# Performance work log

Hardware: AMD Instinct MI355X
Metric: run time of the kernel (lower is better)

## Reference

```python
import jax, jax.numpy as jnp
import numpy as np
import math

B, S, D = 2, 2048, 1024
N_HEAD = 16
EPS = 1e-6

def setup_inputs() -> dict:
    key = jax.random.key(0)
    ks = jax.random.split(key, 12)
    def lin(k):
        kw, kb = jax.random.split(k)
        scale = 1.0 / math.sqrt(D)
        W = jax.random.uniform(kw, (D, D), jnp.float32, -scale, scale)
        b = jax.random.uniform(kb, (D,), jnp.float32, -scale, scale)
        return W, b
    Wq, bq = lin(ks[0]); Wk, bk = lin(ks[1]); Wv, bv = lin(ks[2]); Wo, bo = lin(ks[3])
    return {
        'query': jax.random.normal(ks[4], (B, S, D), jnp.float32),
        'key':   jax.random.normal(ks[5], (B, S, D), jnp.float32),
        'value': jax.random.normal(ks[6], (B, S, D), jnp.float32),
        'mask':  jnp.ones((B, S, S), jnp.int32),
        'Wq': Wq, 'bq': bq, 'Wk': Wk, 'bk': bk, 'Wv': Wv, 'bv': bv,
        'Wo': Wo, 'bo': bo,
        'gamma': jnp.ones((D,), jnp.float32),
        'beta':  jnp.zeros((D,), jnp.float32),
    }

def reference(query, key, value, mask, Wq, bq, Wk, bk, Wv, bv, Wo, bo, gamma, beta):
    b, s, dm = query.shape
    h = N_HEAD
    d = dm // h
    residual = query
    # projections (torch Linear: x @ W.T + b) -> [b, h, s, d]
    def proj(x, W, bias):
        return (x @ W.T + bias).reshape(b, -1, h, d).transpose(0, 2, 1, 3)
    q = proj(query, Wq, bq)
    k = proj(key, Wk, bk)
    v = proj(value, Wv, bv)
    scores = jnp.einsum('bhqd,bhkd->bhqk', q, k) / jnp.sqrt(jnp.float32(d))
    scores = jnp.where(mask[:, None, :, :] == 0, jnp.float32(-1e9), scores)
    p_attn = jax.nn.softmax(scores, axis=-1)  # dropout is identity in eval/reference
    x = jnp.einsum('bhqk,bhkd->bhqd', p_attn, v)
    x = x.transpose(0, 2, 1, 3).reshape(b, -1, h * d)
    x = x @ Wo.T + bo
    x = x + residual
    # LayerNorm with unbiased std and (std + eps) denominator, as in source
    mean = jnp.mean(x, axis=-1, keepdims=True)
    std = jnp.std(x, axis=-1, keepdims=True, ddof=1)
    return gamma * (x - mean) / (std + EPS) + beta
```

## Files before the change

kernel.cpp:

```cpp
#include <hip/hip_runtime.h>
#include <hip/hip_bf16.h>
#include <math.h>
#include <stdint.h>

#define BATCH 2
#define SEQ   2048
#define DMODEL 1024
#define NHEAD 16
#define HDIM  64
#define NROWS (BATCH*SEQ)
#define EPS   1e-6f
#define QSCALE 0.1803368801111204f

typedef float f32x4 __attribute__((ext_vector_type(4)));
typedef short s16x8 __attribute__((ext_vector_type(8)));

#define OFF_XQ 0
#define OFF_XK 4194304
#define OFF_XV 8388608
#define OFF_WQ 12582912
#define OFF_WK 13631488
#define OFF_WV 14680064
#define OFF_WO 15728640
#define OFF_QB 16777216
#define OFF_KB 20971520
#define OFF_VT 25165824
#define OFF_CM 29360128
#define OFF_MS 29884416

__device__ __forceinline__ unsigned short f2bf(float x) {
    unsigned int u = __builtin_bit_cast(unsigned int, x);
    u += 0x7fff + ((u >> 16) & 1);
    return (unsigned short)(u >> 16);
}

__device__ __forceinline__ void gl_lds16(const void* g, void* l) {
    __builtin_amdgcn_global_load_lds(
        (const __attribute__((address_space(1))) unsigned int*)g,
        (__attribute__((address_space(3))) unsigned int*)(unsigned int)(unsigned long long)l,
        16, 0, 0);
}

__global__ __launch_bounds__(256) void conv_all_kernel(
    const float* __restrict__ q, const float* __restrict__ k, const float* __restrict__ v,
    const float* __restrict__ wq, const float* __restrict__ wk, const float* __restrict__ wv,
    const float* __restrict__ wo, unsigned short* __restrict__ ws)
{
    if (blockIdx.x == 0 && threadIdx.x < 32)
        ((unsigned int*)(ws + OFF_MS))[threadIdx.x] = 0;
    size_t t = ((size_t)blockIdx.x * 256 + threadIdx.x) * 4;
    const float* src; unsigned short* dst; size_t off;
    if (t < 4194304)       { src = q;  dst = ws + OFF_XQ; off = t; }
    else if (t < 8388608)  { src = k;  dst = ws + OFF_XK; off = t - 4194304; }
    else if (t < 12582912) { src = v;  dst = ws + OFF_XV; off = t - 8388608; }
    else if (t < 13631488) { src = wq; dst = ws + OFF_WQ; off = t - 12582912; }
    else if (t < 14680064) { src = wk; dst = ws + OFF_WK; off = t - 13631488; }
    else if (t < 15728640) { src = wv; dst = ws + OFF_WV; off = t - 14680064; }
    else                   { src = wo; dst = ws + OFF_WO; off = t - 15728640; }
    float4 x = *(const float4*)&src[off];
    ushort4 o;
    o.x = f2bf(x.x); o.y = f2bf(x.y); o.z = f2bf(x.z); o.w = f2bf(x.w);
    *(ushort4*)&dst[off] = o;
}

__global__ __launch_bounds__(256) void mask_compress_kernel(
    const int* __restrict__ mask, unsigned long long* __restrict__ cm,
    unsigned int* __restrict__ msum)
{
    int t = blockIdx.x * 256 + threadIdx.x;
    int s  = t & 2047;
    int kb = (t >> 11) & 31;
    int b  = t >> 16;
    const int* mp = mask + ((size_t)b * SEQ + s) * SEQ + kb * 64;
    unsigned long long bits = 0;
    #pragma unroll
    for (int i = 0; i < 16; i++) {
        int4 m4 = *(const int4*)&mp[i * 4];
        unsigned long long nib =
            (unsigned long long)((m4.x != 0) | ((m4.y != 0) << 1) |
                                 ((m4.z != 0) << 2) | ((m4.w != 0) << 3));
        bits |= nib << (i * 4);
    }
    cm[((size_t)b * 32 + kb) * SEQ + s] = bits;
    if (bits != ~0ull)
        atomicOr(&msum[(b << 4) | (s >> 7)], 1u << kb);
}

__device__ __forceinline__ void gemm_body(
    const unsigned short* A, const unsigned short* W, int r0, int c0,
    unsigned short* As, unsigned short* Bs, f32x4 acc[4][4])
{
    const int tid  = threadIdx.x;
    const int wave = tid >> 6, lane = tid & 63;
    const int quad = lane >> 4, l15 = lane & 15;
    const int wr = wave >> 1, wc = wave & 1;
    for (int k0 = 0; k0 < DMODEL; k0 += 64) {
        __syncthreads();
        #pragma unroll
        for (int r = 0; r < 4; r++) {
            int f   = r * 4096 + tid * 16;
            int row = f >> 7;
            int g   = (((f >> 4) & 7) - row) & 7;
            gl_lds16((const char*)A + (size_t)(r0 + row) * 2048 + k0 * 2 + g * 16,
                     (char*)As + r * 4096 + wave * 1024);
            gl_lds16((const char*)W + (size_t)(c0 + row) * 2048 + k0 * 2 + g * 16,
                     (char*)Bs + r * 4096 + wave * 1024);
        }
        __syncthreads();
        #pragma unroll
        for (int ks = 0; ks < 2; ks++) {
            s16x8 a[4], b[4];
            #pragma unroll
            for (int mt = 0; mt < 4; mt++) {
                int row = wr*64 + mt*16 + l15;
                a[mt] = *(const s16x8*)((const char*)As + row * 128 + ((ks*4 + quad + row) & 7) * 16);
            }
            #pragma unroll
            for (int nt = 0; nt < 4; nt++) {
                int row = wc*64 + nt*16 + l15;
                b[nt] = *(const s16x8*)((const char*)Bs + row * 128 + ((ks*4 + quad + row) & 7) * 16);
            }
            #pragma unroll
            for (int mt = 0; mt < 4; mt++)
                #pragma unroll
                for (int nt = 0; nt < 4; nt++)
                    acc[mt][nt] = __builtin_amdgcn_mfma_f32_16x16x32_bf16(a[mt], b[nt], acc[mt][nt], 0, 0, 0);
        }
    }
}

__global__ __launch_bounds__(256) void qkv_gemm_kernel(
    unsigned short* __restrict__ ws,
    const float* __restrict__ bq, const float* __restrict__ bk, const float* __restrict__ bv)
{
    __shared__ __align__(16) unsigned short As[8192];
    __shared__ __align__(16) unsigned short Bs[8192];
    const int z = blockIdx.z;
    const unsigned short *A, *W;
    int r0, c0;
    if (z != 2) {
        A = ws + (size_t)z * 4194304;
        W = ws + OFF_WQ + (size_t)z * 1048576;
        r0 = blockIdx.x * 128; c0 = blockIdx.y * 128;
    } else {
        A = ws + OFF_WV;
        W = ws + OFF_XV;
        r0 = blockIdx.y * 128; c0 = blockIdx.x * 128;
    }
    const float* bias = (z == 0) ? bq : (z == 1 ? bk : bv);
    unsigned short* outp = ws + OFF_QB + (size_t)z * 4194304;
    const float scale = (z == 0) ? QSCALE : 1.0f;

    f32x4 acc[4][4] = {};
    gemm_body(A, W, r0, c0, As, Bs, acc);

    const int lane = threadIdx.x & 63, wave = threadIdx.x >> 6;
    const int quad = lane >> 4, l15 = lane & 15;
    const int wr = wave >> 1, wc = wave & 1;
    if (z != 2) {
        float bias_v[4];
        #pragma unroll
        for (int nt = 0; nt < 4; nt++) bias_v[nt] = bias[c0 + wc*64 + nt*16 + l15];
        #pragma unroll
        for (int mt = 0; mt < 4; mt++) {
            #pragma unroll
            for (int nt = 0; nt < 4; nt++) {
                int c = c0 + wc*64 + nt*16 + l15;
                int hh = c >> 6, dd = c & 63;
                #pragma unroll
                for (int reg = 0; reg < 4; reg++) {
                    int r = r0 + wr*64 + mt*16 + quad*4 + reg;
                    int bb = r >> 11, ss = r & (SEQ - 1);
                    float val = (acc[mt][nt][reg] + bias_v[nt]) * scale;
                    outp[(((size_t)(bb*NHEAD + hh)) * SEQ + ss) * HDIM + dd] = f2bf(val);
                }
            }
        }
    } else {
        #pragma unroll
        for (int mt = 0; mt < 4; mt++) {
            #pragma unroll
            for (int reg = 0; reg < 4; reg++) {
                int f = r0 + wr*64 + mt*16 + quad*4 + reg;
                int hh = f >> 6, dd = f & 63;
                float bfv = bias[f];
                #pragma unroll
                for (int nt = 0; nt < 4; nt++) {
                    int r = c0 + wc*64 + nt*16 + l15;
                    int bb = r >> 11, ss = r & (SEQ - 1);
                    outp[(((size_t)(bb*NHEAD + hh)) * HDIM + dd) * SEQ + ss] =
                        f2bf(acc[mt][nt][reg] + bfv);
                }
            }
        }
    }
}

__global__ __launch_bounds__(256) void oproj_gemm_kernel(
    const unsigned short* __restrict__ ws, const float* __restrict__ bo,
    const float* __restrict__ resid, float* __restrict__ outf)
{
    __shared__ __align__(16) unsigned short As[8192];
    __shared__ __align__(16) unsigned short Bs[8192];
    const unsigned short* A = ws + OFF_XQ;
    const unsigned short* W = ws + OFF_WO;
    const int r0 = blockIdx.x * 128, c0 = blockIdx.y * 128;

    f32x4 acc[4][4] = {};
    gemm_body(A, W, r0, c0, (unsigned short*)As, (unsigned short*)Bs, acc);

    const int lane = threadIdx.x & 63, wave = threadIdx.x >> 6;
    const int quad = lane >> 4, l15 = lane & 15;
    const int wr = wave >> 1, wc = wave & 1;
    #pragma unroll
    for (int mt = 0; mt < 4; mt++) {
        #pragma unroll
        for (int nt = 0; nt < 4; nt++) {
            int c = c0 + wc*64 + nt*16 + l15;
            float bv = bo[c];
            #pragma unroll
            for (int reg = 0; reg < 4; reg++) {
                int r = r0 + wr*64 + mt*16 + quad*4 + reg;
                size_t idx = (size_t)r * DMODEL + c;
                outf[idx] = acc[mt][nt][reg] + bv + resid[idx];
            }
        }
    }
}

__global__ __launch_bounds__(512) void attn_mfma_kernel(
    const unsigned short* __restrict__ ws,
    const unsigned long long* __restrict__ cmask,
    const unsigned int* __restrict__ msum,
    unsigned short* __restrict__ ab)
{
    const int tid  = threadIdx.x;
    const int wave = tid >> 6, lane = tid & 63;
    const int quad = lane >> 4, l15 = lane & 15;
    const int h = blockIdx.y, b = blockIdx.z;
    const int qw = blockIdx.x * 128 + wave * 16;

    const char* qh = (const char*)(ws + OFF_QB + ((size_t)(b*NHEAD + h)) * SEQ * HDIM);
    const char* kh = (const char*)(ws + OFF_KB + ((size_t)(b*NHEAD + h)) * SEQ * HDIM);
    const char* vh = (const char*)(ws + OFF_VT + ((size_t)(b*NHEAD + h)) * SEQ * HDIM);

    __shared__ __align__(16) char Ks[2][8192];
    __shared__ __align__(16) char Vs[2][8192];
    __shared__ __align__(16) unsigned short Pl[8][16 * 72];
    unsigned short* Pw = Pl[wave];

    const unsigned int chunkflags = msum[(b << 4) | blockIdx.x];

    const int srow = tid >> 3;
    const int sgrp = ((tid & 7) - srow) & 7;

    #define STAGE(bf, k0)                                                       \
        do {                                                                    \
            gl_lds16(kh + (size_t)((k0) + srow) * 128 + sgrp * 16,              \
                     Ks[bf] + wave * 1024);                                     \
            gl_lds16(vh + (size_t)srow * 4096 + (size_t)(k0) * 2 + sgrp * 16,   \
                     Vs[bf] + wave * 1024);                                     \
        } while (0)

    s16x8 qa[2];
    #pragma unroll
    for (int ks = 0; ks < 2; ks++)
        qa[ks] = *(const s16x8*)(qh + (size_t)(qw + l15) * 128 + ks*64 + quad*16);

    s16x8 onesf;
    {
        short so = (short)0x3F80;
        if (l15 == 0) onesf = (s16x8){so, so, so, so, so, so, so, so};
        else          onesf = (s16x8){0, 0, 0, 0, 0, 0, 0, 0};
    }

    f32x4 o[4], lsum = {0.f, 0.f, 0.f, 0.f};
    #pragma unroll
    for (int nt = 0; nt < 4; nt++) o[nt] = (f32x4){0.f, 0.f, 0.f, 0.f};

    STAGE(0, 0);
    int bf = 0;
    for (int k0 = 0; k0 < SEQ; k0 += 64) {
        __syncthreads();
        if (k0 + 64 < SEQ) STAGE(bf ^ 1, k0 + 64);

        const char* Kb = Ks[bf];
        const char* Vb = Vs[bf];
        f32x4 s[4];
        #pragma unroll
        for (int nt = 0; nt < 4; nt++) {
            int key = nt*16 + l15;
            s16x8 kf0 = *(const s16x8*)(Kb + key*128 + ((quad     + key) & 7) * 16);
            s16x8 kf1 = *(const s16x8*)(Kb + key*128 + ((4 + quad + key) & 7) * 16);
            f32x4 z = {0.f, 0.f, 0.f, 0.f};
            s[nt] = __builtin_amdgcn_mfma_f32_16x16x32_bf16(qa[0], kf0, z, 0, 0, 0);
            s[nt] = __builtin_amdgcn_mfma_f32_16x16x32_bf16(qa[1], kf1, s[nt], 0, 0, 0);
        }
        if (chunkflags & (1u << (k0 >> 6))) {
            const unsigned long long* cmp =
                cmask + ((size_t)b*32 + (k0 >> 6)) * SEQ + qw + quad*4;
            #pragma unroll
            for (int reg = 0; reg < 4; reg++) {
                unsigned long long cm = cmp[reg];
                if (cm != ~0ull) {
                    #pragma unroll
                    for (int nt = 0; nt < 4; nt++) {
                        int n = nt*16 + l15;
                        if (!((cm >> n) & 1)) s[nt][reg] = -1e9f;
                    }
                }
            }
        }
        #pragma unroll
        for (int nt = 0; nt < 4; nt++)
            #pragma unroll
            for (int reg = 0; reg < 4; reg++) {
                float pv = exp2f(s[nt][reg]);
                Pw[(quad*4 + reg) * 72 + nt*16 + l15] =
                    (unsigned short)(__builtin_bit_cast(unsigned int, pv) >> 16);
            }
        #pragma unroll
        for (int ks = 0; ks < 2; ks++) {
            s16x8 pa = *(const s16x8*)((const char*)Pw + l15 * 144 + ks*64 + quad*16);
            lsum = __builtin_amdgcn_mfma_f32_16x16x32_bf16(pa, onesf, lsum, 0, 0, 0);
            #pragma unroll
            for (int nt = 0; nt < 4; nt++) {
                int d = nt*16 + l15;
                s16x8 vf = *(const s16x8*)(Vb + d*128 + ((ks*4 + quad + d) & 7) * 16);
                o[nt] = __builtin_amdgcn_mfma_f32_16x16x32_bf16(pa, vf, o[nt], 0, 0, 0);
            }
        }
        bf ^= 1;
    }
    #undef STAGE
    #pragma unroll
    for (int reg = 0; reg < 4; reg++) {
        float lv = __shfl(lsum[reg], lane & 48);
        float inv = 1.f / lv;
        int sg = qw + quad*4 + reg;
        #pragma unroll
        for (int nt = 0; nt < 4; nt++) {
            size_t idx = ((size_t)b * SEQ + sg) * DMODEL + h*HDIM + nt*16 + l15;
            ab[idx] = f2bf(o[nt][reg] * inv);
        }
    }
}

__global__ __launch_bounds__(256) void ln_kernel(
    float* __restrict__ x, const float* __restrict__ gamma,
    const float* __restrict__ beta)
{
    const int row = blockIdx.x;
    const int tid = threadIdx.x;
    float4 vals = *(const float4*)&x[(size_t)row * DMODEL + tid * 4];
    float s  = vals.x + vals.y + vals.z + vals.w;
    float ss = vals.x*vals.x + vals.y*vals.y + vals.z*vals.z + vals.w*vals.w;
    #pragma unroll
    for (int off = 32; off > 0; off >>= 1) {
        s  += __shfl_down(s, off);
        ss += __shfl_down(ss, off);
    }
    __shared__ float sbuf[4], ssbuf[4];
    __shared__ float mean_s, inv_s;
    if ((tid & 63) == 0) { sbuf[tid >> 6] = s; ssbuf[tid >> 6] = ss; }
    __syncthreads();
    if (tid == 0) {
        float S1 = 0.f, S2 = 0.f;
        #pragma unroll
        for (int i = 0; i < 4; i++) { S1 += sbuf[i]; S2 += ssbuf[i]; }
        float mean = S1 * (1.0f / DMODEL);
        float var  = (S2 - (float)DMODEL * mean * mean) * (1.0f / (DMODEL - 1));
        float sd   = sqrtf(fmaxf(var, 0.f));
        mean_s = mean;
        inv_s  = 1.f / (sd + EPS);
    }
    __syncthreads();
    float4 g  = *(const float4*)&gamma[tid * 4];
    float4 bt = *(const float4*)&beta[tid * 4];
    float4 o;
    o.x = g.x * (vals.x - mean_s) * inv_s + bt.x;
    o.y = g.y * (vals.y - mean_s) * inv_s + bt.y;
    o.z = g.z * (vals.z - mean_s) * inv_s + bt.z;
    o.w = g.w * (vals.w - mean_s) * inv_s + bt.w;
    *(float4*)&x[(size_t)row * DMODEL + tid * 4] = o;
}

extern "C" void kernel_launch(void* const* d_in, const int* in_sizes, int n_in,
                              void* d_out, int out_size, void* d_ws, size_t ws_size,
                              hipStream_t stream) {
    const float* query = (const float*)d_in[0];
    const float* key   = (const float*)d_in[1];
    const float* value = (const float*)d_in[2];
    const int*   mask  = (const int*)d_in[3];
    const float* Wq = (const float*)d_in[4];  const float* bq = (const float*)d_in[5];
    const float* Wk = (const float*)d_in[6];  const float* bk = (const float*)d_in[7];
    const float* Wv = (const float*)d_in[8];  const float* bv = (const float*)d_in[9];
    const float* Wo = (const float*)d_in[10]; const float* bo = (const float*)d_in[11];
    const float* gamma = (const float*)d_in[12];
    const float* beta  = (const float*)d_in[13];
    float* out = (float*)d_out;

    unsigned short* ws = (unsigned short*)d_ws;
    unsigned long long* cmask = (unsigned long long*)(ws + OFF_CM);
    unsigned int* msum = (unsigned int*)(ws + OFF_MS);

    conv_all_kernel<<<16384, 256, 0, stream>>>(query, key, value, Wq, Wk, Wv, Wo, ws);
    mask_compress_kernel<<<512, 256, 0, stream>>>(mask, cmask, msum);
    qkv_gemm_kernel<<<dim3(32, 8, 3), 256, 0, stream>>>(ws, bq, bk, bv);
    attn_mfma_kernel<<<dim3(SEQ/128, NHEAD, BATCH), 512, 0, stream>>>(ws, cmask, msum, ws + OFF_XQ);
    oproj_gemm_kernel<<<dim3(32, 8), 256, 0, stream>>>(ws, bo, query, out);
    ln_kernel<<<NROWS, 256, 0, stream>>>(out, gamma, beta);
}
```

Measured before the change: 281.3 us.

## Process two query tiles per wave in attention to reuse K/V fragments

The attention kernel now runs 4 waves of 256 threads, each handling 32 query rows (two 16-row MFMA tiles) instead of 8 waves with 16 rows each. Each K and V fragment read from LDS feeds two MFMAs, halving LDS reads per MFMA, and the staging code issues twice as many loads per thread to fill the same 64-key tile. In exchange, register pressure per wave roughly doubles, and there are fewer waves per block to hide latency. Launch bounds are changed to request 2 blocks per CU.

```diff
diff --git a/kernel.cpp b/kernel.cpp
--- a/kernel.cpp
+++ b/kernel.cpp
@@ -228,7 +228,7 @@
     }
 }
 
-__global__ __launch_bounds__(512) void attn_mfma_kernel(
+__global__ __launch_bounds__(256, 2) void attn_mfma_kernel(
     const unsigned short* __restrict__ ws,
     const unsigned long long* __restrict__ cmask,
     const unsigned int* __restrict__ msum,
@@ -238,7 +238,7 @@
     const int wave = tid >> 6, lane = tid & 63;
     const int quad = lane >> 4, l15 = lane & 15;
     const int h = blockIdx.y, b = blockIdx.z;
-    const int qw = blockIdx.x * 128 + wave * 16;
+    const int qw = blockIdx.x * 128 + wave * 32;
 
     const char* qh = (const char*)(ws + OFF_QB + ((size_t)(b*NHEAD + h)) * SEQ * HDIM);
     const char* kh = (const char*)(ws + OFF_KB + ((size_t)(b*NHEAD + h)) * SEQ * HDIM);
@@ -246,7 +246,7 @@
 
     __shared__ __align__(16) char Ks[2][8192];
     __shared__ __align__(16) char Vs[2][8192];
-    __shared__ __align__(16) unsigned short Pl[8][16 * 72];
+    __shared__ __align__(16) unsigned short Pl[4][32 * 72];
     unsigned short* Pw = Pl[wave];
 
     const unsigned int chunkflags = msum[(b << 4) | blockIdx.x];
@@ -254,18 +254,24 @@
     const int srow = tid >> 3;
     const int sgrp = ((tid & 7) - srow) & 7;
 
-    #define STAGE(bf, k0)                                                       \
-        do {                                                                    \
-            gl_lds16(kh + (size_t)((k0) + srow) * 128 + sgrp * 16,              \
-                     Ks[bf] + wave * 1024);                                     \
-            gl_lds16(vh + (size_t)srow * 4096 + (size_t)(k0) * 2 + sgrp * 16,   \
-                     Vs[bf] + wave * 1024);                                     \
+    #define STAGE(bf, k0)                                                          \
+        do {                                                                       \
+            gl_lds16(kh + (size_t)((k0) + srow) * 128 + sgrp * 16,                 \
+                     Ks[bf] + wave * 1024);                                        \
+            gl_lds16(kh + (size_t)((k0) + 32 + srow) * 128 + sgrp * 16,            \
+                     Ks[bf] + 4096 + wave * 1024);                                 \
+            gl_lds16(vh + (size_t)srow * 4096 + (size_t)(k0) * 2 + sgrp * 16,      \
+                     Vs[bf] + wave * 1024);                                        \
+            gl_lds16(vh + (size_t)(32 + srow) * 4096 + (size_t)(k0) * 2 + sgrp * 16,\
+                     Vs[bf] + 4096 + wave * 1024);                                 \
         } while (0)
 
-    s16x8 qa[2];
-    #pragma unroll
-    for (int ks = 0; ks < 2; ks++)
-        qa[ks] = *(const s16x8*)(qh + (size_t)(qw + l15) * 128 + ks*64 + quad*16);
+    s16x8 qa[2][2];
+    #pragma unroll
+    for (int m = 0; m < 2; m++)
+        #pragma unroll
+        for (int ks = 0; ks < 2; ks++)
+            qa[m][ks] = *(const s16x8*)(qh + (size_t)(qw + m*16 + l15) * 128 + ks*64 + quad*16);
 
     s16x8 onesf;
     {
@@ -274,9 +280,13 @@
         else          onesf = (s16x8){0, 0, 0, 0, 0, 0, 0, 0};
     }
 
-    f32x4 o[4], lsum = {0.f, 0.f, 0.f, 0.f};
-    #pragma unroll
-    for (int nt = 0; nt < 4; nt++) o[nt] = (f32x4){0.f, 0.f, 0.f, 0.f};
+    f32x4 o[2][4], lsum[2];
+    #pragma unroll
+    for (int m = 0; m < 2; m++) {
+        lsum[m] = (f32x4){0.f, 0.f, 0.f, 0.f};
+        #pragma unroll
+        for (int nt = 0; nt < 4; nt++) o[m][nt] = (f32x4){0.f, 0.f, 0.f, 0.f};
+    }
 
     STAGE(0, 0);
     int bf = 0;
@@ -286,64 +296,77 @@
 
         const char* Kb = Ks[bf];
         const char* Vb = Vs[bf];
-        f32x4 s[4];
+        f32x4 s[2][4];
         #pragma unroll
         for (int nt = 0; nt < 4; nt++) {
             int key = nt*16 + l15;
             s16x8 kf0 = *(const s16x8*)(Kb + key*128 + ((quad     + key) & 7) * 16);
             s16x8 kf1 = *(const s16x8*)(Kb + key*128 + ((4 + quad + key) & 7) * 16);
-            f32x4 z = {0.f, 0.f, 0.f, 0.f};
-            s[nt] = __builtin_amdgcn_mfma_f32_16x16x32_bf16(qa[0], kf0, z, 0, 0, 0);
-            s[nt] = __builtin_amdgcn_mfma_f32_16x16x32_bf16(qa[1], kf1, s[nt], 0, 0, 0);
+            #pragma unroll
+            for (int m = 0; m < 2; m++) {
+                f32x4 z = {0.f, 0.f, 0.f, 0.f};
+                s[m][nt] = __builtin_amdgcn_mfma_f32_16x16x32_bf16(qa[m][0], kf0, z, 0, 0, 0);
+                s[m][nt] = __builtin_amdgcn_mfma_f32_16x16x32_bf16(qa[m][1], kf1, s[m][nt], 0, 0, 0);
+            }
         }
         if (chunkflags & (1u << (k0 >> 6))) {
-            const unsigned long long* cmp =
-                cmask + ((size_t)b*32 + (k0 >> 6)) * SEQ + qw + quad*4;
-            #pragma unroll
-            for (int reg = 0; reg < 4; reg++) {
-                unsigned long long cm = cmp[reg];
-                if (cm != ~0ull) {
-                    #pragma unroll
-                    for (int nt = 0; nt < 4; nt++) {
-                        int n = nt*16 + l15;
-                        if (!((cm >> n) & 1)) s[nt][reg] = -1e9f;
+            #pragma unroll
+            for (int m = 0; m < 2; m++) {
+                const unsigned long long* cmp =
+                    cmask + ((size_t)b*32 + (k0 >> 6)) * SEQ + qw + m*16 + quad*4;
+                #pragma unroll
+                for (int reg = 0; reg < 4; reg++) {
+                    unsigned long long cm = cmp[reg];
+                    if (cm != ~0ull) {
+                        #pragma unroll
+                        for (int nt = 0; nt < 4; nt++) {
+                            int n = nt*16 + l15;
+                            if (!((cm >> n) & 1)) s[m][nt][reg] = -1e9f;
+                        }
                     }
                 }
             }
         }
         #pragma unroll
-        for (int nt = 0; nt < 4; nt++)
-            #pragma unroll
-            for (int reg = 0; reg < 4; reg++) {
-                float pv = exp2f(s[nt][reg]);
-                Pw[(quad*4 + reg) * 72 + nt*16 + l15] =
-                    (unsigned short)(__builtin_bit_cast(unsigned int, pv) >> 16);
-            }
+        for (int m = 0; m < 2; m++)
+            #pragma unroll
+            for (int nt = 0; nt < 4; nt++)
+                #pragma unroll
+                for (int reg = 0; reg < 4; reg++) {
+                    float pv = exp2f(s[m][nt][reg]);
+                    Pw[(m*16 + quad*4 + reg) * 72 + nt*16 + l15] =
+                        (unsigned short)(__builtin_bit_cast(unsigned int, pv) >> 16);
+                }
         #pragma unroll
         for (int ks = 0; ks < 2; ks++) {
-            s16x8 pa = *(const s16x8*)((const char*)Pw + l15 * 144 + ks*64 + quad*16);
-            lsum = __builtin_amdgcn_mfma_f32_16x16x32_bf16(pa, onesf, lsum, 0, 0, 0);
+            s16x8 pa0 = *(const s16x8*)((const char*)Pw + (size_t)l15 * 144 + ks*64 + quad*16);
+            s16x8 pa1 = *(const s16x8*)((const char*)Pw + (size_t)(16 + l15) * 144 + ks*64 + quad*16);
+            lsum[0] = __builtin_amdgcn_mfma_f32_16x16x32_bf16(pa0, onesf, lsum[0], 0, 0, 0);
+            lsum[1] = __builtin_amdgcn_mfma_f32_16x16x32_bf16(pa1, onesf, lsum[1], 0, 0, 0);
             #pragma unroll
             for (int nt = 0; nt < 4; nt++) {
                 int d = nt*16 + l15;
                 s16x8 vf = *(const s16x8*)(Vb + d*128 + ((ks*4 + quad + d) & 7) * 16);
-                o[nt] = __builtin_amdgcn_mfma_f32_16x16x32_bf16(pa, vf, o[nt], 0, 0, 0);
+                o[0][nt] = __builtin_amdgcn_mfma_f32_16x16x32_bf16(pa0, vf, o[0][nt], 0, 0, 0);
+                o[1][nt] = __builtin_amdgcn_mfma_f32_16x16x32_bf16(pa1, vf, o[1][nt], 0, 0, 0);
             }
         }
         bf ^= 1;
     }
     #undef STAGE
     #pragma unroll
-    for (int reg = 0; reg < 4; reg++) {
-        float lv = __shfl(lsum[reg], lane & 48);
-        float inv = 1.f / lv;
-        int sg = qw + quad*4 + reg;
-        #pragma unroll
-        for (int nt = 0; nt < 4; nt++) {
-            size_t idx = ((size_t)b * SEQ + sg) * DMODEL + h*HDIM + nt*16 + l15;
-            ab[idx] = f2bf(o[nt][reg] * inv);
-        }
-    }
+    for (int m = 0; m < 2; m++)
+        #pragma unroll
+        for (int reg = 0; reg < 4; reg++) {
+            float lv = __shfl(lsum[m][reg], lane & 48);
+            float inv = 1.f / lv;
+            int row = qw + m*16 + quad*4 + reg;
+            #pragma unroll
+            for (int nt = 0; nt < 4; nt++) {
+                size_t idx = ((size_t)b * SEQ + row) * DMODEL + h*HDIM + nt*16 + l15;
+                ab[idx] = f2bf(o[m][nt][reg] * inv);
+            }
+        }
 }
 
 __global__ __launch_bounds__(256) void ln_kernel(
@@ -407,7 +430,7 @@
     conv_all_kernel<<<16384, 256, 0, stream>>>(query, key, value, Wq, Wk, Wv, Wo, ws);
     mask_compress_kernel<<<512, 256, 0, stream>>>(mask, cmask, msum);
     qkv_gemm_kernel<<<dim3(32, 8, 3), 256, 0, stream>>>(ws, bq, bk, bv);
-    attn_mfma_kernel<<<dim3(SEQ/128, NHEAD, BATCH), 512, 0, stream>>>(ws, cmask, msum, ws + OFF_XQ);
+    attn_mfma_kernel<<<dim3(SEQ/128, NHEAD, BATCH), 256, 0, stream>>>(ws, cmask, msum, ws + OFF_XQ);
     oproj_gemm_kernel<<<dim3(32, 8), 256, 0, stream>>>(ws, bo, query, out);
     ln_kernel<<<NROWS, 256, 0, stream>>>(out, gamma, beta);
 }
```

Result: no change. 285.7 us (+1.6%).
